# Performance work log

Hardware: AMD Instinct MI355X
Metric: run time of the kernel (lower is better)

Reference implementation:

```python
import jax, jax.numpy as jnp
import numpy as np

FIELD = 32
DIM = 64
LAYER_SIZE = (128, 128)


def setup_inputs() -> dict:
    key = jax.random.key(0)
    ks = jax.random.split(key, 5)
    B = 4096
    x = jax.random.normal(ks[0], (B, FIELD, DIM), dtype=jnp.float32)
    # conv1d kernel-size-1 weights, stored as [out_channels, in_channels]
    field_nums = [FIELD]
    params = {}
    for i, size in enumerate(LAYER_SIZE):
        in_ch = field_nums[-1] * field_nums[0]
        fan = 1.0 / np.sqrt(in_ch)
        params[f"w{i}"] = jax.random.uniform(ks[1 + 2 * i % 4], (size, in_ch), minval=-fan, maxval=fan, dtype=jnp.float32)
        params[f"b{i}"] = jax.random.uniform(ks[2 + 2 * i % 4], (size,), minval=-fan, maxval=fan, dtype=jnp.float32)
        field_nums.append(size // 2)
    return {"cin_inputs": x, "w0": params["w0"], "b0": params["b0"], "w1": params["w1"], "b1": params["b1"]}


def _cin(x, weights, biases):
    # x: [B, F, D]
    B, F, D = x.shape
    hidden = x
    finals = []
    n_layers = len(weights)
    for i, (w, b) in enumerate(zip(weights, biases)):
        size = w.shape[0]
        # outer product over field dims: [B, H, F, D] -> reshape to [B, H*F, D]
        z = jnp.einsum('bhd,bfd->bhfd', hidden, x).reshape(B, hidden.shape[1] * F, D)
        # 1x1 conv over channel dim == per-position matmul
        y = jnp.einsum('bcd,oc->bod', z, w) + b[None, :, None]
        y = jax.nn.relu(y)
        if i != n_layers - 1:
            hidden, direct = y[:, : size // 2, :], y[:, size // 2 :, :]
        else:
            direct = y
        finals.append(direct)
    return jnp.concatenate(finals, axis=1).sum(-1)  # [B, out_dim]


def reference(cin_inputs, w0, b0, w1, b1):
    return _cin(cin_inputs, [w0, w1], [b0, b1])
```

## Files before the change

kernel.cpp:

```cpp
#include <hip/hip_runtime.h>
#include <hip/hip_fp16.h>


typedef __attribute__((ext_vector_type(8))) _Float16 f16x8;
typedef __attribute__((ext_vector_type(4))) float f32x4;
typedef __attribute__((ext_vector_type(4))) unsigned short us4;
typedef unsigned short ushortT;

__device__ __forceinline__ int hidx(int o, int d) {
    return o * 64 + (d ^ ((o & 7) << 3));
}

__global__ void cin_pack_w(const float* __restrict__ w0,
                           const float* __restrict__ w1,
                           ushortT* __restrict__ wp) {
    int gidx = blockIdx.x * 256 + threadIdx.x;
    if (gidx >= 49152) return;
    const float* src;
    ushortT* dst;
    if (gidx < 16384) {
        int kk = gidx >> 9, rem = gidx & 511;
        int n = rem >> 6, lp = rem & 63;
        int o = n * 16 + (lp & 15);
        int c = kk * 32 + ((lp >> 4) << 3);
        src = w0 + o * 1024 + c;
        dst = wp + gidx * 8;
    } else {
        int g1 = gidx - 16384;
        int kk = g1 >> 9, rem = g1 & 511;
        int n = rem >> 6, lp = rem & 63;
        int o = n * 16 + (lp & 15);
        int c = kk * 32 + ((lp >> 4) << 3);
        src = w1 + o * 2048 + c;
        dst = wp + 131072 + g1 * 8;
    }
    ushortT tmp[8];
#pragma unroll
    for (int j = 0; j < 8; ++j) {
        __half h = __float2half(src[j]);
        tmp[j] = __builtin_bit_cast(ushortT, h);
    }
    *reinterpret_cast<f16x8*>(dst) = *reinterpret_cast<const f16x8*>(tmp);
}

__global__ __launch_bounds__(256, 2) void cin_mfma_kernel(
    const float* __restrict__ x,
    const float* __restrict__ b0,
    const float* __restrict__ b1,
    const ushortT* __restrict__ wp,
    float* __restrict__ out)
{
    const int tid = threadIdx.x;
    const int l   = tid & 63;
    const int w   = tid >> 6;
    const int b   = blockIdx.x * 4 + w;
    const int r16 = l & 15;
    const int g   = l >> 4;

    __shared__ ushortT U[4][4096];
    __shared__ __align__(16) ushortT Wb[2][4096];

    ushortT* Xw = U[w];

    const float* xb = x + (size_t)b * 2048;
#pragma unroll
    for (int i = 0; i < 8; ++i) {
        float4 v = reinterpret_cast<const float4*>(xb)[i * 64 + l];
        int flat = (i * 64 + l) * 4;
        us4 h;
        h[0] = __builtin_bit_cast(ushortT, __float2half(v.x));
        h[1] = __builtin_bit_cast(ushortT, __float2half(v.y));
        h[2] = __builtin_bit_cast(ushortT, __float2half(v.z));
        h[3] = __builtin_bit_cast(ushortT, __float2half(v.w));
        *reinterpret_cast<us4*>(&Xw[flat]) = h;
    }

    {
        const char* src = (const char*)wp + (size_t)(w * 2) * 1024 + (size_t)l * 16;
        __builtin_amdgcn_global_load_lds((const unsigned int*)src,
                                         (unsigned int*)&Wb[0][(w * 2) * 512], 16, 0, 0);
        __builtin_amdgcn_global_load_lds((const unsigned int*)(src + 1024),
                                         (unsigned int*)&Wb[0][(w * 2 + 1) * 512], 16, 0, 0);
    }
    __syncthreads();

    __half2 tf16[4][4];
#pragma unroll
    for (int mt = 0; mt < 4; ++mt)
#pragma unroll
        for (int p = 0; p < 4; ++p) {
            unsigned lo = Xw[(g * 8 + 2 * p) * 64 + mt * 16 + r16];
            unsigned hi = Xw[(g * 8 + 2 * p + 1) * 64 + mt * 16 + r16];
            tf16[mt][p] = __builtin_bit_cast(__half2, lo | (hi << 16));
        }

    f32x4 acc[4][8];
#pragma unroll
    for (int mt = 0; mt < 4; ++mt)
#pragma unroll
        for (int n = 0; n < 8; ++n) acc[mt][n] = (f32x4){0.f, 0.f, 0.f, 0.f};

    union AfU { __half2 h2[4]; f16x8 v; };

    __half2 thc[4];
#pragma unroll
    for (int mt = 0; mt < 4; ++mt) {
        unsigned u = Xw[mt * 16 + r16];
        thc[mt] = __builtin_bit_cast(__half2, (u << 16) | u);
    }

#pragma unroll 1
    for (int p = 0; p < 96; ++p) {
        const int ps = p & 1;

        if (p + 1 < 96) {
            const char* src = (const char*)wp + (size_t)(p + 1) * 8192 +
                              (size_t)(w * 2) * 1024 + (size_t)l * 16;
            __builtin_amdgcn_global_load_lds((const unsigned int*)src,
                (unsigned int*)&Wb[ps ^ 1][(w * 2) * 512], 16, 0, 0);
            __builtin_amdgcn_global_load_lds((const unsigned int*)(src + 1024),
                (unsigned int*)&Wb[ps ^ 1][(w * 2 + 1) * 512], 16, 0, 0);
        }

        f16x8 Bf[8];
#pragma unroll
        for (int n = 0; n < 8; ++n)
            Bf[n] = *reinterpret_cast<const f16x8*>(&Wb[ps][n * 512 + l * 8]);

        AfU Af[4];
#pragma unroll
        for (int mt = 0; mt < 4; ++mt)
#pragma unroll
            for (int q = 0; q < 4; ++q)
                Af[mt].h2[q] = __hmul2(tf16[mt][q], thc[mt]);

        if (p + 1 < 96) {
            const int kn = p + 1;
#pragma unroll
            for (int mt = 0; mt < 4; ++mt) {
                const int c = mt * 16 + r16;
                unsigned u = (kn < 32) ? Xw[kn * 64 + c]
                                       : Xw[hidx(kn - 32, c)];
                thc[mt] = __builtin_bit_cast(__half2, (u << 16) | u);
            }
        }

        __builtin_amdgcn_s_setprio(1);
#pragma unroll
        for (int n = 0; n < 8; ++n)
#pragma unroll
            for (int mt = 0; mt < 4; ++mt)
                acc[mt][n] = __builtin_amdgcn_mfma_f32_16x16x32_f16(
                    Af[mt].v, Bf[n], acc[mt][n], 0, 0, 0);
        __builtin_amdgcn_s_setprio(0);

        __syncthreads();

        if (p == 31) {
            ushortT* Hw = Xw;
#pragma unroll
            for (int n = 0; n < 4; ++n) {
                float bn = b0[n * 16 + r16];
                const int o = n * 16 + r16;
#pragma unroll
                for (int mt = 0; mt < 4; ++mt) {
                    us4 hv;
#pragma unroll
                    for (int r = 0; r < 4; ++r) {
                        float y = fmaxf(acc[mt][n][r] + bn, 0.f);
                        hv[r] = __builtin_bit_cast(ushortT, __float2half(y));
                    }
                    *reinterpret_cast<us4*>(&Hw[hidx(o, mt * 16 + g * 4)]) = hv;
                }
            }
#pragma unroll
            for (int n = 4; n < 8; ++n) {
                float bn = b0[n * 16 + r16];
                float s = 0.f;
#pragma unroll
                for (int mt = 0; mt < 4; ++mt)
#pragma unroll
                    for (int r = 0; r < 4; ++r)
                        s += fmaxf(acc[mt][n][r] + bn, 0.f);
                s += __shfl_xor(s, 16);
                s += __shfl_xor(s, 32);
                if (l < 16) out[(size_t)b * 192 + (n - 4) * 16 + l] = s;
            }
#pragma unroll
            for (int mt = 0; mt < 4; ++mt)
#pragma unroll
                for (int n = 0; n < 8; ++n) acc[mt][n] = (f32x4){0.f, 0.f, 0.f, 0.f};
#pragma unroll
            for (int mt = 0; mt < 4; ++mt) {
                unsigned u = Hw[hidx(0, mt * 16 + r16)];
                thc[mt] = __builtin_bit_cast(__half2, (u << 16) | u);
            }
        }
    }

#pragma unroll
    for (int n = 0; n < 8; ++n) {
        float bn = b1[n * 16 + r16];
        float s = 0.f;
#pragma unroll
        for (int mt = 0; mt < 4; ++mt)
#pragma unroll
            for (int r = 0; r < 4; ++r)
                s += fmaxf(acc[mt][n][r] + bn, 0.f);
        s += __shfl_xor(s, 16);
        s += __shfl_xor(s, 32);
        if (l < 16) out[(size_t)b * 192 + 64 + n * 16 + l] = s;
    }
}

__global__ __launch_bounds__(256, 4) void cin_fp32_kernel(
    const float* __restrict__ x, const float* __restrict__ w0,
    const float* __restrict__ b0, const float* __restrict__ w1,
    const float* __restrict__ b1, float* __restrict__ out)
{
    const int b = blockIdx.x;
    const int tid = threadIdx.x;
    const int d = tid & 63;
    const int wave = tid >> 6;

    __shared__ float Xs[32][64];
    __shared__ float Hsf[64][64];

    const float* xb = x + (size_t)b * 2048;
    float treg[32];
#pragma unroll
    for (int f = 0; f < 32; ++f) treg[f] = xb[f * 64 + d];
    if (wave == 0) {
#pragma unroll
        for (int f = 0; f < 32; ++f) Xs[f][d] = treg[f];
    }
    __syncthreads();
    const int o_base = __builtin_amdgcn_readfirstlane(wave * 32);

    for (int oi = 0; oi < 32; ++oi) {
        const int o = o_base + oi;
        const float* wrow = w0 + (size_t)o * 1024;
        float acc = b0[o];
        for (int h = 0; h < 32; ++h) {
            const float* wv = wrow + h * 32;
            const float th = Xs[h][d];
            float s0 = 0.f, s1 = 0.f, s2 = 0.f, s3 = 0.f;
#pragma unroll
            for (int f = 0; f < 32; f += 4) {
                s0 = fmaf(wv[f + 0], treg[f + 0], s0);
                s1 = fmaf(wv[f + 1], treg[f + 1], s1);
                s2 = fmaf(wv[f + 2], treg[f + 2], s2);
                s3 = fmaf(wv[f + 3], treg[f + 3], s3);
            }
            acc = fmaf((s0 + s1) + (s2 + s3), th, acc);
        }
        float y = fmaxf(acc, 0.f);
        if (o < 64) {
            Hsf[o][d] = y;
        } else {
#pragma unroll
            for (int off = 32; off > 0; off >>= 1) y += __shfl_xor(y, off, 64);
            if (d == 0) out[(size_t)b * 192 + (o - 64)] = y;
        }
    }
    __syncthreads();

    for (int oi = 0; oi < 32; ++oi) {
        const int o = o_base + oi;
        const float* wrow = w1 + (size_t)o * 2048;
        float acc = b1[o];
        for (int h = 0; h < 64; ++h) {
            const float* wv = wrow + h * 32;
            const float th = Hsf[h][d];
            float s0 = 0.f, s1 = 0.f, s2 = 0.f, s3 = 0.f;
#pragma unroll
            for (int f = 0; f < 32; f += 4) {
                s0 = fmaf(wv[f + 0], treg[f + 0], s0);
                s1 = fmaf(wv[f + 1], treg[f + 1], s1);
                s2 = fmaf(wv[f + 2], treg[f + 2], s2);
                s3 = fmaf(wv[f + 3], treg[f + 3], s3);
            }
            acc = fmaf((s0 + s1) + (s2 + s3), th, acc);
        }
        float y = fmaxf(acc, 0.f);
#pragma unroll
        for (int off = 32; off > 0; off >>= 1) y += __shfl_xor(y, off, 64);
        if (d == 0) out[(size_t)b * 192 + 64 + o] = y;
    }
}

extern "C" void kernel_launch(void* const* d_in, const int* in_sizes, int n_in,
                              void* d_out, int out_size, void* d_ws, size_t ws_size,
                              hipStream_t stream) {
    const float* x  = (const float*)d_in[0];
    const float* w0 = (const float*)d_in[1];
    const float* b0 = (const float*)d_in[2];
    const float* w1 = (const float*)d_in[3];
    const float* b1 = (const float*)d_in[4];
    float* out = (float*)d_out;

    if (ws_size >= 786432) {
        ushortT* wp = (ushortT*)d_ws;
        cin_pack_w<<<192, 256, 0, stream>>>(w0, w1, wp);
        cin_mfma_kernel<<<1024, 256, 0, stream>>>(x, b0, b1, wp, out);
    } else {
        cin_fp32_kernel<<<4096, 256, 0, stream>>>(x, w0, b0, w1, b1, out);
    }
}
```

Baseline: 174.2 us.

## Stage three weight K-slices per barrier and split loop at layer boundary

Each pipeline stage now loads three 8 KB weight slices into a larger LDS double buffer, so one __syncthreads covers three MFMA bursts instead of one. The 96-step loop is split into an x-phase loop, a peeled transition step that writes the hidden layer, and an h-phase loop, which removes the per-iteration p==31 and kn<32 branches. Each burst also builds the A fragment per mt right before its MFMAs, which should lower register pressure. The cost is three times more LDS for weights (48 KB total for Wb), which may reduce occupancy at two blocks per CU.

```diff
diff --git a/kernel.cpp b/kernel.cpp
--- a/kernel.cpp
+++ b/kernel.cpp
@@ -43,6 +43,56 @@
     *reinterpret_cast<f16x8*>(dst) = *reinterpret_cast<const f16x8*>(tmp);
 }
 
+#define LOAD_TH_X(K, DST)                                           \
+    _Pragma("unroll")                                               \
+    for (int mt = 0; mt < 4; ++mt) {                                \
+        unsigned u = Xw[(K) * 64 + mt * 16 + r16];                  \
+        (DST)[mt] = __builtin_bit_cast(__half2, (u << 16) | u);     \
+    }
+
+#define LOAD_TH_H(K, DST)                                           \
+    _Pragma("unroll")                                               \
+    for (int mt = 0; mt < 4; ++mt) {                                \
+        unsigned u = Xw[hidx((K) - 32, mt * 16 + r16)];             \
+        (DST)[mt] = __builtin_bit_cast(__half2, (u << 16) | u);     \
+    }
+
+#define COPY_TH(DST, SRC)                                           \
+    _Pragma("unroll")                                               \
+    for (int mt = 0; mt < 4; ++mt) (DST)[mt] = (SRC)[mt];
+
+#define BURST(WBASE, TH)                                            \
+    {                                                               \
+        f16x8 Bf[8];                                                \
+        _Pragma("unroll")                                           \
+        for (int n = 0; n < 8; ++n)                                 \
+            Bf[n] = *reinterpret_cast<const f16x8*>(                \
+                &(WBASE)[n * 512 + l * 8]);                         \
+        __builtin_amdgcn_s_setprio(1);                              \
+        _Pragma("unroll")                                           \
+        for (int mt = 0; mt < 4; ++mt) {                            \
+            AfU Af;                                                 \
+            _Pragma("unroll")                                       \
+            for (int q = 0; q < 4; ++q)                             \
+                Af.h2[q] = __hmul2(tf16[mt][q], (TH)[mt]);          \
+            _Pragma("unroll")                                       \
+            for (int n = 0; n < 8; ++n)                             \
+                acc[mt][n] = __builtin_amdgcn_mfma_f32_16x16x32_f16(\
+                    Af.v, Bf[n], acc[mt][n], 0, 0, 0);              \
+        }                                                           \
+        __builtin_amdgcn_s_setprio(0);                              \
+    }
+
+#define STAGE_TRIPLE(T, SLOT)                                       \
+    _Pragma("unroll")                                               \
+    for (int j = 0; j < 6; ++j) {                                   \
+        const int seg = w * 6 + j;                                  \
+        const char* src = (const char*)wp + (size_t)(T) * 24576 +   \
+                          (size_t)seg * 1024 + (size_t)l * 16;      \
+        __builtin_amdgcn_global_load_lds((const unsigned int*)src,  \
+            (unsigned int*)&Wb[SLOT][seg * 512], 16, 0, 0);         \
+    }
+
 __global__ __launch_bounds__(256, 2) void cin_mfma_kernel(
     const float* __restrict__ x,
     const float* __restrict__ b0,
@@ -58,7 +108,7 @@
     const int g   = l >> 4;
 
     __shared__ ushortT U[4][4096];
-    __shared__ __align__(16) ushortT Wb[2][4096];
+    __shared__ __align__(16) ushortT Wb[2][12288];
 
     ushortT* Xw = U[w];
 
@@ -75,13 +125,7 @@
         *reinterpret_cast<us4*>(&Xw[flat]) = h;
     }
 
-    {
-        const char* src = (const char*)wp + (size_t)(w * 2) * 1024 + (size_t)l * 16;
-        __builtin_amdgcn_global_load_lds((const unsigned int*)src,
-                                         (unsigned int*)&Wb[0][(w * 2) * 512], 16, 0, 0);
-        __builtin_amdgcn_global_load_lds((const unsigned int*)(src + 1024),
-                                         (unsigned int*)&Wb[0][(w * 2 + 1) * 512], 16, 0, 0);
-    }
+    STAGE_TRIPLE(0, 0);
     __syncthreads();
 
     __half2 tf16[4][4];
@@ -102,100 +146,102 @@
 
     union AfU { __half2 h2[4]; f16x8 v; };
 
-    __half2 thc[4];
-#pragma unroll
-    for (int mt = 0; mt < 4; ++mt) {
-        unsigned u = Xw[mt * 16 + r16];
-        thc[mt] = __builtin_bit_cast(__half2, (u << 16) | u);
-    }
+    __half2 thA[4], thB[4];
+    LOAD_TH_X(0, thA);
 
 #pragma unroll 1
-    for (int p = 0; p < 96; ++p) {
+    for (int p = 0; p < 10; ++p) {
         const int ps = p & 1;
-
-        if (p + 1 < 96) {
-            const char* src = (const char*)wp + (size_t)(p + 1) * 8192 +
-                              (size_t)(w * 2) * 1024 + (size_t)l * 16;
-            __builtin_amdgcn_global_load_lds((const unsigned int*)src,
-                (unsigned int*)&Wb[ps ^ 1][(w * 2) * 512], 16, 0, 0);
-            __builtin_amdgcn_global_load_lds((const unsigned int*)(src + 1024),
-                (unsigned int*)&Wb[ps ^ 1][(w * 2 + 1) * 512], 16, 0, 0);
-        }
-
-        f16x8 Bf[8];
-#pragma unroll
-        for (int n = 0; n < 8; ++n)
-            Bf[n] = *reinterpret_cast<const f16x8*>(&Wb[ps][n * 512 + l * 8]);
-
-        AfU Af[4];
+        const int k0 = 3 * p;
+
+        STAGE_TRIPLE(p + 1, ps ^ 1);
+
+        LOAD_TH_X(k0 + 1, thB);
+        BURST(&Wb[ps][0], thA);
+        COPY_TH(thA, thB);
+
+        LOAD_TH_X(k0 + 2, thB);
+        BURST(&Wb[ps][4096], thA);
+        COPY_TH(thA, thB);
+
+        LOAD_TH_X(k0 + 3, thB);
+        BURST(&Wb[ps][8192], thA);
+        COPY_TH(thA, thB);
+
+        __syncthreads();
+    }
+
+    {
+        STAGE_TRIPLE(11, 1);
+
+        LOAD_TH_X(31, thB);
+        BURST(&Wb[0][0], thA);
+        COPY_TH(thA, thB);
+
+        BURST(&Wb[0][4096], thA);
+
+        ushortT* Hw = Xw;
+#pragma unroll
+        for (int n = 0; n < 4; ++n) {
+            float bn = b0[n * 16 + r16];
+            const int o = n * 16 + r16;
+#pragma unroll
+            for (int mt = 0; mt < 4; ++mt) {
+                us4 hv;
+#pragma unroll
+                for (int r = 0; r < 4; ++r) {
+                    float y = fmaxf(acc[mt][n][r] + bn, 0.f);
+                    hv[r] = __builtin_bit_cast(ushortT, __float2half(y));
+                }
+                *reinterpret_cast<us4*>(&Hw[hidx(o, mt * 16 + g * 4)]) = hv;
+            }
+        }
+#pragma unroll
+        for (int n = 4; n < 8; ++n) {
+            float bn = b0[n * 16 + r16];
+            float s = 0.f;
+#pragma unroll
+            for (int mt = 0; mt < 4; ++mt)
+#pragma unroll
+                for (int r = 0; r < 4; ++r)
+                    s += fmaxf(acc[mt][n][r] + bn, 0.f);
+            s += __shfl_xor(s, 16);
+            s += __shfl_xor(s, 32);
+            if (l < 16) out[(size_t)b * 192 + (n - 4) * 16 + l] = s;
+        }
 #pragma unroll
         for (int mt = 0; mt < 4; ++mt)
 #pragma unroll
-            for (int q = 0; q < 4; ++q)
-                Af[mt].h2[q] = __hmul2(tf16[mt][q], thc[mt]);
-
-        if (p + 1 < 96) {
-            const int kn = p + 1;
-#pragma unroll
-            for (int mt = 0; mt < 4; ++mt) {
-                const int c = mt * 16 + r16;
-                unsigned u = (kn < 32) ? Xw[kn * 64 + c]
-                                       : Xw[hidx(kn - 32, c)];
-                thc[mt] = __builtin_bit_cast(__half2, (u << 16) | u);
-            }
-        }
-
-        __builtin_amdgcn_s_setprio(1);
-#pragma unroll
-        for (int n = 0; n < 8; ++n)
-#pragma unroll
-            for (int mt = 0; mt < 4; ++mt)
-                acc[mt][n] = __builtin_amdgcn_mfma_f32_16x16x32_f16(
-                    Af[mt].v, Bf[n], acc[mt][n], 0, 0, 0);
-        __builtin_amdgcn_s_setprio(0);
+            for (int n = 0; n < 8; ++n) acc[mt][n] = (f32x4){0.f, 0.f, 0.f, 0.f};
+
+        LOAD_TH_H(32, thA);
+        LOAD_TH_H(33, thB);
+        BURST(&Wb[0][8192], thA);
+        COPY_TH(thA, thB);
 
         __syncthreads();
-
-        if (p == 31) {
-            ushortT* Hw = Xw;
-#pragma unroll
-            for (int n = 0; n < 4; ++n) {
-                float bn = b0[n * 16 + r16];
-                const int o = n * 16 + r16;
-#pragma unroll
-                for (int mt = 0; mt < 4; ++mt) {
-                    us4 hv;
-#pragma unroll
-                    for (int r = 0; r < 4; ++r) {
-                        float y = fmaxf(acc[mt][n][r] + bn, 0.f);
-                        hv[r] = __builtin_bit_cast(ushortT, __float2half(y));
-                    }
-                    *reinterpret_cast<us4*>(&Hw[hidx(o, mt * 16 + g * 4)]) = hv;
-                }
-            }
-#pragma unroll
-            for (int n = 4; n < 8; ++n) {
-                float bn = b0[n * 16 + r16];
-                float s = 0.f;
-#pragma unroll
-                for (int mt = 0; mt < 4; ++mt)
-#pragma unroll
-                    for (int r = 0; r < 4; ++r)
-                        s += fmaxf(acc[mt][n][r] + bn, 0.f);
-                s += __shfl_xor(s, 16);
-                s += __shfl_xor(s, 32);
-                if (l < 16) out[(size_t)b * 192 + (n - 4) * 16 + l] = s;
-            }
-#pragma unroll
-            for (int mt = 0; mt < 4; ++mt)
-#pragma unroll
-                for (int n = 0; n < 8; ++n) acc[mt][n] = (f32x4){0.f, 0.f, 0.f, 0.f};
-#pragma unroll
-            for (int mt = 0; mt < 4; ++mt) {
-                unsigned u = Hw[hidx(0, mt * 16 + r16)];
-                thc[mt] = __builtin_bit_cast(__half2, (u << 16) | u);
-            }
-        }
+    }
+
+#pragma unroll 1
+    for (int p = 11; p < 32; ++p) {
+        const int ps = p & 1;
+        const int k0 = 3 * p;
+
+        if (p + 1 < 32) { STAGE_TRIPLE(p + 1, ps ^ 1); }
+
+        LOAD_TH_H(k0 + 1, thB);
+        BURST(&Wb[ps][0], thA);
+        COPY_TH(thA, thB);
+
+        LOAD_TH_H(k0 + 2, thB);
+        BURST(&Wb[ps][4096], thA);
+        COPY_TH(thA, thB);
+
+        if (p + 1 < 32) { LOAD_TH_H(k0 + 3, thB); }
+        BURST(&Wb[ps][8192], thA);
+        COPY_TH(thA, thB);
+
+        __syncthreads();
     }
 
 #pragma unroll
```

Measured after the change: 183.6 us. +5.4%, slower.
